# Kernel optimization log

Measured on AMD Instinct MI355X. Metric: run time of the kernel, lower is better.

The kernel has to match this reference:

```python
import jax, jax.numpy as jnp
import numpy as np

FS = 4096.0
TRAIN_KERNEL = 4
TRAIN_STRIDE = 0.25
BATCH = 1024
NPERSEG = 4096          # fftlength * fs
NOVERLAP = NPERSEG // 2 # default overlap
FL, FH = 20.0, 500.0


def _welch(data):
    """Faithful port of _torch_welch with average='mean' (which is a SUM over segments
    in the original code), off by the same constant factor as the original."""
    N, nsample = data.shape
    nstride = NPERSEG - NOVERLAP
    nseg = int(np.ceil((nsample - NPERSEG) / nstride)) + 1
    # frame indices [nseg, nperseg] (static numpy -> cheap gather)
    idx = np.arange(nseg)[:, None] * nstride + np.arange(NPERSEG)[None, :]
    frames = data[:, idx]                                   # [N, nseg, nperseg]
    n = np.arange(NPERSEG)
    window = (0.5 - 0.5 * np.cos(2.0 * np.pi * n / NPERSEG)).astype(np.float32) * 2.0  # periodic hann * 2
    fd = jnp.fft.rfft(frames * window, axis=-1)             # [N, nseg, nfreq]
    power = jnp.real(fd) ** 2 + jnp.imag(fd) ** 2
    psd = jnp.sum(power, axis=1)                            # original 'mean' branch uses sum
    T = nsample * FS
    return psd / T                                          # [N, nfreq]


def setup_inputs() -> dict:
    key = jax.random.key(0)
    k1, k2 = jax.random.split(key)
    T = int(TRAIN_KERNEL * FS)  # 16384
    pred = jax.random.normal(k1, (BATCH, T), dtype=jnp.float32)
    target = jax.random.normal(k2, (BATCH, T), dtype=jnp.float32)
    return {"pred": pred, "target": target}


def reference(pred, target):
    res = target - pred
    s = int(TRAIN_STRIDE * FS)                     # 1024 samples per stride
    shape_x = int(TRAIN_KERNEL / TRAIN_STRIDE)     # 16
    # cross[i] = res[:, i*s:(i+1)*s].flatten() -> reshape/transpose, no loop
    def to_cross(x):
        return x[:, : shape_x * s].reshape(BATCH, shape_x, s).transpose(1, 0, 2).reshape(shape_x, BATCH * s)
    cross_res = to_cross(res)
    cross_target = to_cross(target)

    psd_res = _welch(cross_res)                    # [shape_x, nfreq]
    psd_target = _welch(cross_target)

    nfreq = NPERSEG // 2 + 1
    freq = np.linspace(0.0, FS / 2.0, nfreq)
    mask = jnp.asarray((FL < freq) & (freq < FH))
    dfreq = float(freq[1] - freq[0])
    scale = FH - FL

    psd_res = jnp.where(mask, psd_res, 0.0)
    psd_ratio = psd_res / psd_target
    loss = jnp.sum(psd_ratio, axis=1) * dfreq / scale  # [shape_x]
    return jnp.mean(loss[-8:]) * loss.shape[0]
```

## Files before the change

kernel.cpp:

```cpp
#include <hip/hip_runtime.h>

#define NSEG 511
#define NROWS 8
#define ROW0 8
#define K0 21
#define KEND 500
#define NFREQ 479
#define ACC_STRIDE 512
#define ACC_ELEMS (2 * NROWS * ACC_STRIDE)
#define NREP 8
#define SPB 4
#define NGROUPS 128
#define NBLOCKS (2 * NROWS * NGROUPS)

__device__ __forceinline__ int sw(int i) { return i ^ (((i >> 5) & 7) << 2); }
__device__ __forceinline__ int ms(int m) { return m ^ ((m >> 6) & 7); }

__device__ __forceinline__ float2 cmul(float2 a, float2 b) {
    return make_float2(fmaf(a.x, b.x, -a.y * b.y), fmaf(a.x, b.y, a.y * b.x));
}
__device__ __forceinline__ float2 cadd(float2 a, float2 b) { return make_float2(a.x + b.x, a.y + b.y); }
__device__ __forceinline__ float2 csub(float2 a, float2 b) { return make_float2(a.x - b.x, a.y - b.y); }

__device__ __forceinline__ void dft8(float2& x0, float2& x1, float2& x2, float2& x3,
                                     float2& x4, float2& x5, float2& x6, float2& x7) {
    const float C45 = 0.70710678118654752440f;
    float2 t0 = cadd(x0, x4), u0 = csub(x0, x4);
    float2 t1 = cadd(x1, x5), u1 = csub(x1, x5);
    float2 t2 = cadd(x2, x6), u2 = csub(x2, x6);
    float2 t3 = cadd(x3, x7), u3 = csub(x3, x7);
    float2 s0 = cadd(t0, t2), d0 = csub(t0, t2);
    float2 s1 = cadd(t1, t3), d1 = csub(t1, t3);
    float2 v1 = make_float2(C45 * (u1.x + u1.y), C45 * (u1.y - u1.x));
    float2 v2 = make_float2(u2.y, -u2.x);
    float2 v3 = make_float2(C45 * (u3.y - u3.x), -C45 * (u3.x + u3.y));
    float2 s2 = cadd(u0, v2), d2 = csub(u0, v2);
    float2 s3 = cadd(v1, v3), d3 = csub(v1, v3);
    float2 mid1 = make_float2(d1.y, -d1.x);
    float2 mid3 = make_float2(d3.y, -d3.x);
    x0 = cadd(s0, s1); x4 = csub(s0, s1);
    x2 = cadd(d0, mid1); x6 = csub(d0, mid1);
    x1 = cadd(s2, s3); x5 = csub(s2, s3);
    x3 = cadd(d2, mid3); x7 = csub(d2, mid3);
}

__device__ __forceinline__ void twiddle8cs(float2& x1, float2& x2, float2& x3, float2& x4,
                                           float2& x5, float2& x6, float2& x7,
                                           float c, float s) {
    float2 w1 = make_float2(c, s);
    float2 w2 = cmul(w1, w1);
    float2 w3 = cmul(w2, w1);
    float2 w4 = cmul(w2, w2);
    float2 w5 = cmul(w4, w1);
    float2 w6 = cmul(w3, w3);
    float2 w7 = cmul(w4, w3);
    x1 = cmul(x1, w1); x2 = cmul(x2, w2); x3 = cmul(x3, w3);
    x4 = cmul(x4, w4); x5 = cmul(x5, w5); x6 = cmul(x6, w6);
    x7 = cmul(x7, w7);
}

__global__ __launch_bounds__(256)
void psd_kernel(const float* __restrict__ pred,
                const float* __restrict__ target,
                float* __restrict__ acc) {
    __shared__ float2 buf[2048];
    __shared__ float2 nat[1024];

    const int bid = blockIdx.x;
    const int grp = bid % NGROUPS;
    const int row = (bid / NGROUPS) % NROWS + ROW0;
    const int sig = bid / (NGROUPS * NROWS);
    const int tid = threadIdx.x;
    const int seg0 = grp * SPB;
    const int ns = (seg0 + SPB <= NSEG) ? SPB : (NSEG - seg0);
    float* accR = acc + (bid & (NREP - 1)) * ACC_ELEMS;

    const float2* t2p = (const float2*)target;
    const float2* p2p = (const float2*)pred;

    const int base = 2 * seg0 * 8192 + row * 512 + tid;
#define LOADRAW(X, IDX)                                                      \
    {                                                                        \
        int _i = (IDX);                                                      \
        float2 v = t2p[_i];                                                  \
        if (sig == 0) { float2 p = p2p[_i]; v.x -= p.x; v.y -= p.y; }        \
        X = v;                                                               \
    }
    float2 r0, r1, r2, r3, r4, r5, r6, r7;
    LOADRAW(r0, base)
    LOADRAW(r1, base + 256)
    LOADRAW(r2, base + 8192)
    LOADRAW(r3, base + 8448)
    LOADRAW(r4, base + 16384)
    LOADRAW(r5, base + 16640)
    LOADRAW(r6, base + 24576)
    LOADRAW(r7, base + 24832)

    const float WA = 3.06796157577128245e-3f;
    const float CD = 0.99999882344642529f;
    const float SD = 1.53398018628476550e-3f;
    const float H  = 0.70710678118654752440f;
    float sa, ca;
    __sincosf((float)tid * WA, &sa, &ca);
    float2 wv0, wv1, wv2, wv3, wv4, wv5, wv6, wv7;
#define MKW(W, CE, SE) { float cr = (CE), sr = (SE);                         \
        W = make_float2(1.0f - cr, 1.0f - (cr * CD - sr * SD)); }
    MKW(wv0, ca, sa)
    MKW(wv1, H * (ca - sa), H * (sa + ca))
    MKW(wv2, -sa, ca)
    MKW(wv3, -H * (ca + sa), H * (ca - sa))
    MKW(wv4, -ca, -sa)
    MKW(wv5, H * (sa - ca), -H * (sa + ca))
    MKW(wv6, sa, -ca)
    MKW(wv7, H * (ca + sa), H * (sa - ca))
#undef MKW
    float sb, cb;
    __sincosf((float)(tid & 31) * -2.45436926061702596e-2f, &sb, &cb);
    float cc, ss;
    {
        const float TC1 = 0.98078528040323044913f, TS1 = -0.19509032201612826785f;
        const float TC2 = 0.92387953251128675613f, TS2 = -0.38268343236508977173f;
        const float TC3 = 0.83146961230254523708f, TS3 = -0.55557023301960222474f;
        int mq = tid & 3;
        cc = (mq & 2) ? ((mq & 1) ? TC3 : TC2) : ((mq & 1) ? TC1 : 1.0f);
        ss = (mq & 2) ? ((mq & 1) ? TS3 : TS2) : ((mq & 1) ? TS1 : 0.0f);
    }
    float sn0, cs0, sn1, cs1;
    __sincosf(-1.53398078788564123e-3f * (float)(K0 + tid), &sn0, &cs0);
    {
        const float CU = 0.98078528040323044913f;
        const float SU = 0.19509032201612826785f;
        cs1 = cs0 * CU + sn0 * SU;
        sn1 = sn0 * CU - cs0 * SU;
    }

    float pw1 = 0.0f, pw2 = 0.0f;
    float4* b4 = (float4*)buf;

    #pragma unroll 1
    for (int s = 0; s < ns; ++s) {
        float2 x0 = make_float2(r0.x * wv0.x, r0.y * wv0.y);
        float2 x1 = make_float2(r1.x * wv1.x, r1.y * wv1.y);
        float2 x2 = make_float2(r2.x * wv2.x, r2.y * wv2.y);
        float2 x3 = make_float2(r3.x * wv3.x, r3.y * wv3.y);
        float2 x4 = make_float2(r4.x * wv4.x, r4.y * wv4.y);
        float2 x5 = make_float2(r5.x * wv5.x, r5.y * wv5.y);
        float2 x6 = make_float2(r6.x * wv6.x, r6.y * wv6.y);
        float2 x7 = make_float2(r7.x * wv7.x, r7.y * wv7.y);

        if (s + 1 < ns) {
            r0 = r4; r1 = r5; r2 = r6; r3 = r7;
            int nb = base + (s + 1) * 16384;
            LOADRAW(r4, nb + 16384)
            LOADRAW(r5, nb + 16640)
            LOADRAW(r6, nb + 24576)
            LOADRAW(r7, nb + 24832)
        }

        dft8(x0, x1, x2, x3, x4, x5, x6, x7);
        twiddle8cs(x1, x2, x3, x4, x5, x6, x7, ca, -sa);
        buf[sw(tid)]        = x0;
        buf[sw(tid + 256)]  = x1;
        buf[sw(tid + 512)]  = x2;
        buf[sw(tid + 768)]  = x3;
        buf[sw(tid + 1024)] = x4;
        buf[sw(tid + 1280)] = x5;
        buf[sw(tid + 1536)] = x6;
        buf[sw(tid + 1792)] = x7;
        __syncthreads();

        {
            const int baseB = (tid & 31) + 256 * (tid >> 5);
            x0 = buf[sw(baseB)];
            x1 = buf[sw(baseB + 32)];
            x2 = buf[sw(baseB + 64)];
            x3 = buf[sw(baseB + 96)];
            x4 = buf[sw(baseB + 128)];
            x5 = buf[sw(baseB + 160)];
            x6 = buf[sw(baseB + 192)];
            x7 = buf[sw(baseB + 224)];
            dft8(x0, x1, x2, x3, x4, x5, x6, x7);
            twiddle8cs(x1, x2, x3, x4, x5, x6, x7, cb, sb);
            buf[sw(baseB)]       = x0;
            buf[sw(baseB + 32)]  = x1;
            buf[sw(baseB + 64)]  = x2;
            buf[sw(baseB + 96)]  = x3;
            buf[sw(baseB + 128)] = x4;
            buf[sw(baseB + 160)] = x5;
            buf[sw(baseB + 192)] = x6;
            buf[sw(baseB + 224)] = x7;
        }
        __syncthreads();

        {
            const int baseC = (tid & 3) + 32 * ((tid >> 2) & 7) + 256 * (tid >> 5);
            x0 = buf[sw(baseC)];
            x1 = buf[sw(baseC + 4)];
            x2 = buf[sw(baseC + 8)];
            x3 = buf[sw(baseC + 12)];
            x4 = buf[sw(baseC + 16)];
            x5 = buf[sw(baseC + 20)];
            x6 = buf[sw(baseC + 24)];
            x7 = buf[sw(baseC + 28)];
            dft8(x0, x1, x2, x3, x4, x5, x6, x7);
            twiddle8cs(x1, x2, x3, x4, x5, x6, x7, cc, ss);
            buf[sw(baseC)]      = x0;
            buf[sw(baseC + 4)]  = x1;
            buf[sw(baseC + 8)]  = x2;
            buf[sw(baseC + 12)] = x3;
            buf[sw(baseC + 16)] = x4;
            buf[sw(baseC + 20)] = x5;
            buf[sw(baseC + 24)] = x6;
            buf[sw(baseC + 28)] = x7;
        }
        __syncthreads();

#define QUAD(N)                                                              \
        {                                                                    \
            int n = (N);                                                     \
            int q4 = sw(4 * n) >> 1;                                         \
            float4 lo = b4[q4], hi = b4[q4 + 1];                             \
            float2 X0 = make_float2((lo.x + hi.x) + (lo.z + hi.z),           \
                                    (lo.y + hi.y) + (lo.w + hi.w));          \
            float D0x = lo.x - hi.x, D0y = lo.y - hi.y;                      \
            float D1x = lo.z - hi.z, D1y = lo.w - hi.w;                      \
            float2 X3 = make_float2(D0x - D1y, D0y + D1x);                   \
            int m = 64 * (n & 7) + 8 * ((n >> 3) & 7) + (n >> 6);            \
            int a = ms(m);                                                   \
            nat[a] = X0;                                                     \
            nat[512 + a] = X3;                                               \
        }
        QUAD(tid)
        QUAD(tid + 256)
#undef QUAD
        __syncthreads();

        {
            int k = K0 + tid;
            float2 zk = nat[ms(k)];
            float2 zn = nat[512 + ms(512 - k)];
            float Ex = 0.5f * (zk.x + zn.x);
            float Ey = 0.5f * (zk.y - zn.y);
            float Ox = 0.5f * (zk.y + zn.y);
            float Oy = -0.5f * (zk.x - zn.x);
            float xr = Ex + Ox * cs0 - Oy * sn0;
            float xi = Ey + Ox * sn0 + Oy * cs0;
            pw1 += xr * xr + xi * xi;
        }
        if (tid < KEND - K0 - 256) {
            int k = K0 + 256 + tid;
            float2 zk = nat[ms(k)];
            float2 zn = nat[512 + ms(512 - k)];
            float Ex = 0.5f * (zk.x + zn.x);
            float Ey = 0.5f * (zk.y - zn.y);
            float Ox = 0.5f * (zk.y + zn.y);
            float Oy = -0.5f * (zk.x - zn.x);
            float xr = Ex + Ox * cs1 - Oy * sn1;
            float xi = Ey + Ox * sn1 + Oy * cs1;
            pw2 += xr * xr + xi * xi;
        }
        __syncthreads();
    }

    {
        int i0 = (sig * NROWS + (row - ROW0)) * ACC_STRIDE;
        atomicAdd(&accR[i0 + tid], pw1);
        if (tid < KEND - K0 - 256) atomicAdd(&accR[i0 + 256 + tid], pw2);
    }
#undef LOADRAW
}

__global__ __launch_bounds__(256)
void reduce_kernel(const float* __restrict__ acc, float* __restrict__ out) {
    __shared__ float sh[256];
    int tid = threadIdx.x;
    float sum = 0.0f;
    for (int n = tid; n < NROWS * NFREQ; n += 256) {
        int r = n / NFREQ, k = n % NFREQ;
        float num = 0.0f, den = 0.0f;
        #pragma unroll
        for (int rep = 0; rep < NREP; ++rep) {
            num += acc[rep * ACC_ELEMS + r * ACC_STRIDE + k];
            den += acc[rep * ACC_ELEMS + (NROWS + r) * ACC_STRIDE + k];
        }
        sum += num / den;
    }
    sh[tid] = sum;
    __syncthreads();
    for (int s = 128; s > 0; s >>= 1) {
        if (tid < s) sh[tid] += sh[tid + s];
        __syncthreads();
    }
    if (tid == 0) out[0] = sh[0] * (1.0f / 240.0f);
}

extern "C" void kernel_launch(void* const* d_in, const int* in_sizes, int n_in,
                              void* d_out, int out_size, void* d_ws, size_t ws_size,
                              hipStream_t stream) {
    const float* pred = (const float*)d_in[0];
    const float* target = (const float*)d_in[1];
    float* acc = (float*)d_ws;

    hipMemsetAsync(acc, 0, NREP * ACC_ELEMS * sizeof(float), stream);
    psd_kernel<<<NBLOCKS, 256, 0, stream>>>(pred, target, acc);
    reduce_kernel<<<1, 256, 0, stream>>>(acc, (float*)d_out);
}
```

Baseline: 168.8 us.

## Halve segments per block, drop nat LDS buffer, recompute window in loop

Each block now handles 2 segments instead of 4, which doubles the grid, and the kernel requests 8 blocks per SM through launch bounds. The separate 8 KB 'nat' shared array is removed: the final radix stage reads into registers, syncs, then writes back into buf. Window coefficients, stage twiddles and the second-half rotation are recomputed inside the loop instead of being held in registers. The aim is to cut LDS and VGPR use so more blocks fit per CU, at the cost of an extra barrier, more ALU work per segment, and more atomics and input reloads from the doubled grid.

```diff
diff --git a/kernel.cpp b/kernel.cpp
--- a/kernel.cpp
+++ b/kernel.cpp
@@ -9,8 +9,8 @@
 #define ACC_STRIDE 512
 #define ACC_ELEMS (2 * NROWS * ACC_STRIDE)
 #define NREP 8
-#define SPB 4
-#define NGROUPS 128
+#define SPB 2
+#define NGROUPS 256
 #define NBLOCKS (2 * NROWS * NGROUPS)
 
 __device__ __forceinline__ int sw(int i) { return i ^ (((i >> 5) & 7) << 2); }
@@ -59,12 +59,11 @@
     x7 = cmul(x7, w7);
 }
 
-__global__ __launch_bounds__(256)
+__global__ __launch_bounds__(256, 8)
 void psd_kernel(const float* __restrict__ pred,
                 const float* __restrict__ target,
                 float* __restrict__ acc) {
     __shared__ float2 buf[2048];
-    __shared__ float2 nat[1024];
 
     const int bid = blockIdx.x;
     const int grp = bid % NGROUPS;
@@ -97,56 +96,35 @@
     LOADRAW(r7, base + 24832)
 
     const float WA = 3.06796157577128245e-3f;
-    const float CD = 0.99999882344642529f;
-    const float SD = 1.53398018628476550e-3f;
-    const float H  = 0.70710678118654752440f;
     float sa, ca;
     __sincosf((float)tid * WA, &sa, &ca);
-    float2 wv0, wv1, wv2, wv3, wv4, wv5, wv6, wv7;
-#define MKW(W, CE, SE) { float cr = (CE), sr = (SE);                         \
-        W = make_float2(1.0f - cr, 1.0f - (cr * CD - sr * SD)); }
-    MKW(wv0, ca, sa)
-    MKW(wv1, H * (ca - sa), H * (sa + ca))
-    MKW(wv2, -sa, ca)
-    MKW(wv3, -H * (ca + sa), H * (ca - sa))
-    MKW(wv4, -ca, -sa)
-    MKW(wv5, H * (sa - ca), -H * (sa + ca))
-    MKW(wv6, sa, -ca)
-    MKW(wv7, H * (ca + sa), H * (sa - ca))
-#undef MKW
     float sb, cb;
     __sincosf((float)(tid & 31) * -2.45436926061702596e-2f, &sb, &cb);
-    float cc, ss;
-    {
-        const float TC1 = 0.98078528040323044913f, TS1 = -0.19509032201612826785f;
-        const float TC2 = 0.92387953251128675613f, TS2 = -0.38268343236508977173f;
-        const float TC3 = 0.83146961230254523708f, TS3 = -0.55557023301960222474f;
-        int mq = tid & 3;
-        cc = (mq & 2) ? ((mq & 1) ? TC3 : TC2) : ((mq & 1) ? TC1 : 1.0f);
-        ss = (mq & 2) ? ((mq & 1) ? TS3 : TS2) : ((mq & 1) ? TS1 : 0.0f);
-    }
-    float sn0, cs0, sn1, cs1;
+    float sn0, cs0;
     __sincosf(-1.53398078788564123e-3f * (float)(K0 + tid), &sn0, &cs0);
-    {
-        const float CU = 0.98078528040323044913f;
-        const float SU = 0.19509032201612826785f;
-        cs1 = cs0 * CU + sn0 * SU;
-        sn1 = sn0 * CU - cs0 * SU;
-    }
 
     float pw1 = 0.0f, pw2 = 0.0f;
     float4* b4 = (float4*)buf;
 
     #pragma unroll 1
     for (int s = 0; s < ns; ++s) {
-        float2 x0 = make_float2(r0.x * wv0.x, r0.y * wv0.y);
-        float2 x1 = make_float2(r1.x * wv1.x, r1.y * wv1.y);
-        float2 x2 = make_float2(r2.x * wv2.x, r2.y * wv2.y);
-        float2 x3 = make_float2(r3.x * wv3.x, r3.y * wv3.y);
-        float2 x4 = make_float2(r4.x * wv4.x, r4.y * wv4.y);
-        float2 x5 = make_float2(r5.x * wv5.x, r5.y * wv5.y);
-        float2 x6 = make_float2(r6.x * wv6.x, r6.y * wv6.y);
-        float2 x7 = make_float2(r7.x * wv7.x, r7.y * wv7.y);
+        const float CD = 0.99999882344642529f;
+        const float SD = 1.53398018628476550e-3f;
+        const float H  = 0.70710678118654752440f;
+        float2 x0, x1, x2, x3, x4, x5, x6, x7;
+#define WINR(X, RV, CE, SE)                                                  \
+        { float cr = (CE), sr = (SE);                                        \
+          X = make_float2(RV.x * (1.0f - cr),                                \
+                          RV.y * (1.0f - (cr * CD - sr * SD))); }
+        WINR(x0, r0, ca, sa)
+        WINR(x1, r1, H * (ca - sa), H * (sa + ca))
+        WINR(x2, r2, -sa, ca)
+        WINR(x3, r3, -H * (ca + sa), H * (ca - sa))
+        WINR(x4, r4, -ca, -sa)
+        WINR(x5, r5, H * (sa - ca), -H * (sa + ca))
+        WINR(x6, r6, sa, -ca)
+        WINR(x7, r7, H * (ca + sa), H * (sa - ca))
+#undef WINR
 
         if (s + 1 < ns) {
             r0 = r4; r1 = r5; r2 = r6; r3 = r7;
@@ -203,7 +181,13 @@
             x6 = buf[sw(baseC + 24)];
             x7 = buf[sw(baseC + 28)];
             dft8(x0, x1, x2, x3, x4, x5, x6, x7);
-            twiddle8cs(x1, x2, x3, x4, x5, x6, x7, cc, ss);
+            const float TC1 = 0.98078528040323044913f, TS1 = -0.19509032201612826785f;
+            const float TC2 = 0.92387953251128675613f, TS2 = -0.38268343236508977173f;
+            const float TC3 = 0.83146961230254523708f, TS3 = -0.55557023301960222474f;
+            int mq = tid & 3;
+            float cc = (mq & 2) ? ((mq & 1) ? TC3 : TC2) : ((mq & 1) ? TC1 : 1.0f);
+            float ssv = (mq & 2) ? ((mq & 1) ? TS3 : TS2) : ((mq & 1) ? TS1 : 0.0f);
+            twiddle8cs(x1, x2, x3, x4, x5, x6, x7, cc, ssv);
             buf[sw(baseC)]      = x0;
             buf[sw(baseC + 4)]  = x1;
             buf[sw(baseC + 8)]  = x2;
@@ -215,30 +199,33 @@
         }
         __syncthreads();
 
-#define QUAD(N)                                                              \
-        {                                                                    \
-            int n = (N);                                                     \
-            int q4 = sw(4 * n) >> 1;                                         \
-            float4 lo = b4[q4], hi = b4[q4 + 1];                             \
-            float2 X0 = make_float2((lo.x + hi.x) + (lo.z + hi.z),           \
-                                    (lo.y + hi.y) + (lo.w + hi.w));          \
-            float D0x = lo.x - hi.x, D0y = lo.y - hi.y;                      \
-            float D1x = lo.z - hi.z, D1y = lo.w - hi.w;                      \
-            float2 X3 = make_float2(D0x - D1y, D0y + D1x);                   \
-            int m = 64 * (n & 7) + 8 * ((n >> 3) & 7) + (n >> 6);            \
-            int a = ms(m);                                                   \
-            nat[a] = X0;                                                     \
-            nat[512 + a] = X3;                                               \
-        }
-        QUAD(tid)
-        QUAD(tid + 256)
-#undef QUAD
+        {
+            int q1 = sw(4 * tid) >> 1;
+            int q2 = sw(4 * (tid + 256)) >> 1;
+            float4 lo1 = b4[q1], hi1 = b4[q1 + 1];
+            float4 lo2 = b4[q2], hi2 = b4[q2 + 1];
+            __syncthreads();
+            int m1 = 64 * (tid & 7) + 8 * ((tid >> 3) & 7) + (tid >> 6);
+            int m2 = m1 + (((tid + 256) >> 6) - (tid >> 6));
+            m2 = 64 * ((tid + 256) & 7) + 8 * (((tid + 256) >> 3) & 7) + ((tid + 256) >> 6);
+            float2 X0a = make_float2((lo1.x + hi1.x) + (lo1.z + hi1.z),
+                                     (lo1.y + hi1.y) + (lo1.w + hi1.w));
+            float2 X3a = make_float2((lo1.x - hi1.x) - (lo1.w - hi1.w),
+                                     (lo1.y - hi1.y) + (lo1.z - hi1.z));
+            float2 X0b = make_float2((lo2.x + hi2.x) + (lo2.z + hi2.z),
+                                     (lo2.y + hi2.y) + (lo2.w + hi2.w));
+            float2 X3b = make_float2((lo2.x - hi2.x) - (lo2.w - hi2.w),
+                                     (lo2.y - hi2.y) + (lo2.z - hi2.z));
+            int a1 = ms(m1), a2 = ms(m2);
+            buf[a1] = X0a;  buf[512 + a1] = X3a;
+            buf[a2] = X0b;  buf[512 + a2] = X3b;
+        }
         __syncthreads();
 
         {
             int k = K0 + tid;
-            float2 zk = nat[ms(k)];
-            float2 zn = nat[512 + ms(512 - k)];
+            float2 zk = buf[ms(k)];
+            float2 zn = buf[512 + ms(512 - k)];
             float Ex = 0.5f * (zk.x + zn.x);
             float Ey = 0.5f * (zk.y - zn.y);
             float Ox = 0.5f * (zk.y + zn.y);
@@ -248,9 +235,13 @@
             pw1 += xr * xr + xi * xi;
         }
         if (tid < KEND - K0 - 256) {
+            const float CU = 0.98078528040323044913f;
+            const float SU = 0.19509032201612826785f;
+            float cs1 = cs0 * CU + sn0 * SU;
+            float sn1 = sn0 * CU - cs0 * SU;
             int k = K0 + 256 + tid;
-            float2 zk = nat[ms(k)];
-            float2 zn = nat[512 + ms(512 - k)];
+            float2 zk = buf[ms(k)];
+            float2 zn = buf[512 + ms(512 - k)];
             float Ex = 0.5f * (zk.x + zn.x);
             float Ey = 0.5f * (zk.y - zn.y);
             float Ox = 0.5f * (zk.y + zn.y);
```

Result: slower. 363.1 us (+115.1%).
